# Performance work log

Measured on AMD Instinct MI355X. Metric: run time of the kernel, lower is better.

## Reference

```python
import jax, jax.numpy as jnp
from jax import lax
import numpy as np

START = 1  # strings_utils.SpecialSymbol.START
B, T, H, V = 16, 256, 512, 32000


def setup_inputs() -> dict:
    key = jax.random.key(0)
    ks = jax.random.split(key, 8)
    s = 0.05
    return {
        "hidden0": jax.random.normal(ks[0], (1, B, H), jnp.float32),
        "target": jax.random.randint(ks[1], (B, T), 0, V, jnp.int32),
        "E": jax.random.normal(ks[2], (V, H), jnp.float32) * s,
        "W_ih": jax.random.normal(ks[3], (3 * H, H), jnp.float32) * s,
        "W_hh": jax.random.normal(ks[4], (3 * H, H), jnp.float32) * s,
        "b_ih": jax.random.normal(ks[5], (3 * H,), jnp.float32) * s,
        "b_hh": jax.random.normal(ks[6], (3 * H,), jnp.float32) * s,
        "b_out": jax.random.normal(ks[7], (V,), jnp.float32) * s,
    }


def reference(hidden0, target, E, W_ih, W_hh, b_ih, b_hh, b_out):
    # Teacher forcing: step 0 feeds START, step di>0 feeds target[:, di-1]
    b, t = target.shape
    start = jnp.full((b, 1), START, dtype=target.dtype)
    step_tok = jnp.concatenate([start, target[:, :-1]], axis=1).T  # [T, B]
    h0 = hidden0[0]  # num_layers == 1 -> [B, H]

    def step(h, tok):
        x = E[tok]                                # [B, H] embedding gather
        gi = x @ W_ih.T + b_ih                    # [B, 3H]
        gh = h @ W_hh.T + b_hh                    # [B, 3H]
        i_r, i_z, i_n = jnp.split(gi, 3, axis=-1)
        h_r, h_z, h_n = jnp.split(gh, 3, axis=-1)
        r = jax.nn.sigmoid(i_r + h_r)
        z = jax.nn.sigmoid(i_z + h_z)
        n = jnp.tanh(i_n + r * h_n)
        h_new = (1.0 - z) * n + z * h             # [B, H]
        logits = h_new @ E.T + b_out              # tied-weight output [B, V]
        return h_new, logits

    _, logits = lax.scan(step, h0, step_tok)      # [T, B, V]
    return jnp.transpose(logits, (1, 0, 2))       # [B, T, V]
```

## Files before the change

kernel.cpp:

```cpp
#include <hip/hip_runtime.h>
#include <hip/hip_bf16.h>
#include <math.h>

#define Bq 16
#define Tq 256
#define Hq 512
#define Vq 32000
#define Gq 1536
#define NWG 16
#define LBLK 240
#define NBI 167

typedef __attribute__((ext_vector_type(8))) short short8;
typedef __attribute__((ext_vector_type(4))) float f32x4;
typedef __attribute__((ext_vector_type(4))) unsigned int u32x4;
typedef unsigned long long u64;

typedef const __attribute__((address_space(1))) void g_void;
typedef __attribute__((address_space(3))) void l_void;

__device__ __forceinline__ unsigned short f2bf(float f) {
    union { float f; unsigned int u; } v; v.f = f;
    unsigned int r = v.u + 0x7fffu + ((v.u >> 16) & 1u);
    return (unsigned short)(r >> 16);
}
__device__ __forceinline__ float bf2f(unsigned short h) {
    union { unsigned int u; float f; } v; v.u = ((unsigned int)h) << 16;
    return v.f;
}
__device__ __forceinline__ float sigm(float x) { return 1.0f / (1.0f + __expf(-x)); }
__device__ __forceinline__ float tanh_fast(float x) {
    float e = __expf(-2.0f * x);
    return (1.0f - e) / (1.0f + e);
}

__global__ void prep_kernel(const float* __restrict__ E, const float* __restrict__ Wih,
                            const float* __restrict__ Whh,
                            unsigned short* __restrict__ Ebf,
                            unsigned short* __restrict__ WihHi, unsigned short* __restrict__ WihLo,
                            unsigned short* __restrict__ WhhHi, unsigned short* __restrict__ WhhLo,
                            int* __restrict__ flags) {
    long tid = (long)blockIdx.x * blockDim.x + threadIdx.x;
    long stride = (long)gridDim.x * blockDim.x;
    for (long i = tid; i < (long)Vq * Hq; i += stride) Ebf[i] = f2bf(E[i]);
    for (long i = tid; i < (long)Gq * Hq; i += stride) {
        float w = Wih[i]; unsigned short hi = f2bf(w);
        WihHi[i] = hi; WihLo[i] = f2bf(w - bf2f(hi));
        w = Whh[i]; hi = f2bf(w);
        WhhHi[i] = hi; WhhLo[i] = f2bf(w - bf2f(hi));
    }
    if (tid < 2048) flags[tid] = 0;
}

__launch_bounds__(384)
__global__ void gi_kernel(const int* __restrict__ target, const float* __restrict__ E,
                          const unsigned short* __restrict__ WihHi,
                          const unsigned short* __restrict__ WihLo,
                          const float* __restrict__ b_ih, float* __restrict__ gi_all) {
    __shared__ __align__(16) unsigned short Ahi[16][520];
    __shared__ __align__(16) unsigned short Alo[16][520];
    __shared__ int toks[16];
    int t = blockIdx.x, gb = blockIdx.y;
    int tid = threadIdx.x;
    if (tid < 16) toks[tid] = (t == 0) ? 1 : target[tid * Tq + (t - 1)];
    __syncthreads();
    for (int idx = tid; idx < 16 * Hq; idx += 384) {
        int r = idx >> 9, k = idx & 511;
        float v = E[(long)toks[r] * Hq + k];
        unsigned short hi = f2bf(v);
        Ahi[r][k] = hi; Alo[r][k] = f2bf(v - bf2f(hi));
    }
    __syncthreads();
    int wave = tid >> 6, lane = tid & 63;
    int gcb = gb * 96 + wave * 16;
    int row = lane & 15, kg = (lane >> 4) * 8;
    const unsigned short* bh = WihHi + (long)(gcb + row) * Hq;
    const unsigned short* bl = WihLo + (long)(gcb + row) * Hq;
    f32x4 aHH = {0,0,0,0}, aHL = {0,0,0,0}, aLH = {0,0,0,0};
#pragma unroll
    for (int ks = 0; ks < 16; ++ks) {
        int k0 = ks * 32 + kg;
        short8 ah = *(const short8*)&Ahi[row][k0];
        short8 al = *(const short8*)&Alo[row][k0];
        short8 wh = *(const short8*)&bh[k0];
        short8 wl = *(const short8*)&bl[k0];
        aHH = __builtin_amdgcn_mfma_f32_16x16x32_bf16(ah, wh, aHH, 0, 0, 0);
        aHL = __builtin_amdgcn_mfma_f32_16x16x32_bf16(ah, wl, aHL, 0, 0, 0);
        aLH = __builtin_amdgcn_mfma_f32_16x16x32_bf16(al, wh, aLH, 0, 0, 0);
    }
    int g = gcb + row;
    float bi = b_ih[g];
#pragma unroll
    for (int q = 0; q < 4; ++q) {
        int b = (lane >> 4) * 4 + q;
        gi_all[((long)(t * 16 + b)) * Gq + g] = aHH[q] + aHL[q] + aLH[q] + bi;
    }
}

__launch_bounds__(384, 1)
__global__ void fused_kernel(const float* __restrict__ h0,
                             const unsigned short* __restrict__ WhhHi,
                             const unsigned short* __restrict__ WhhLo,
                             const float* __restrict__ b_hh,
                             const float* __restrict__ gi_all,
                             unsigned int* Hpk, u64* ring,
                             int* flags,
                             const unsigned short* __restrict__ Ebf,
                             const float* __restrict__ b_out,
                             float* __restrict__ out) {
    __shared__ __align__(16) char smem[41984];
    int tid = threadIdx.x, lane = tid & 63;

    if (blockIdx.x < NWG) {
        __builtin_amdgcn_s_setprio(1);
        unsigned short (*Ahi)[520] = (unsigned short (*)[520])smem;
        float (*gbuf)[16][33] = (float (*)[16][33])(smem + 16640);
        int w = blockIdx.x;
        int wave = tid >> 6;
        int gate = wave >> 1;
        int gcol = gate * 512 + w * 32 + (wave & 1) * 16;
        int row = lane & 15, kg = (lane >> 4) * 8;
        const unsigned short* bhp = WhhHi + (long)(gcol + row) * Hq;
        const unsigned short* blp = WhhLo + (long)(gcol + row) * Hq;
        short8 Bh[16], Bl[16];
#pragma unroll
        for (int ks = 0; ks < 16; ++ks) {
            Bh[ks] = *(const short8*)&bhp[ks * 32 + kg];
            Bl[ks] = *(const short8*)&blp[ks * 32 + kg];
        }
        float bhh = b_hh[gcol + row];
        float gin[4];
#pragma unroll
        for (int q = 0; q < 4; ++q) {
            int b = (lane >> 4) * 4 + q;
            gin[q] = gi_all[(long)b * Gq + (gcol + row)];
        }
        for (int t = 0; t < Tq; ++t) {
            if (t == 0) {
                for (int idx = tid; idx < Bq * Hq; idx += 384)
                    Ahi[idx >> 9][idx & 511] = f2bf(h0[idx]);
            } else {
                const u64* src = ring + ((t - 1) & 1) * 4096;
                u64 A0 = (u64)(src + tid);
                u64 A1 = (u64)(src + tid + 384);
                u64 A2 = (u64)(src + tid + 768);
                u64 A3 = (u64)(src + tid + 1152);
                u64 A4 = (u64)(src + tid + 1536);
                u64 A5 = (u64)(src + tid + 1920);
                u64 A6 = (u64)(src + tid + 2304);
                u64 A7 = (u64)(src + tid + 2688);
                u64 A8 = (u64)(src + tid + 3072);
                u64 A9 = (u64)(src + tid + 3456);
                u64 A10 = (u64)(src + ((tid < 256) ? (3840 + tid) : tid));
                u64 v0, v1, v2, v3, v4, v5, v6, v7, v8, v9, v10;
                unsigned int st = (unsigned int)t;
                int guard = 0;
                bool ok;
                do {
                    asm volatile(
                        "global_load_dwordx2 %0, %11, off sc0 sc1\n\t"
                        "global_load_dwordx2 %1, %12, off sc0 sc1\n\t"
                        "global_load_dwordx2 %2, %13, off sc0 sc1\n\t"
                        "global_load_dwordx2 %3, %14, off sc0 sc1\n\t"
                        "global_load_dwordx2 %4, %15, off sc0 sc1\n\t"
                        "global_load_dwordx2 %5, %16, off sc0 sc1\n\t"
                        "global_load_dwordx2 %6, %17, off sc0 sc1\n\t"
                        "global_load_dwordx2 %7, %18, off sc0 sc1\n\t"
                        "global_load_dwordx2 %8, %19, off sc0 sc1\n\t"
                        "global_load_dwordx2 %9, %20, off sc0 sc1\n\t"
                        "global_load_dwordx2 %10, %21, off sc0 sc1\n\t"
                        "s_waitcnt vmcnt(0)"
                        : "=&v"(v0), "=&v"(v1), "=&v"(v2), "=&v"(v3), "=&v"(v4),
                          "=&v"(v5), "=&v"(v6), "=&v"(v7), "=&v"(v8), "=&v"(v9),
                          "=&v"(v10)
                        : "v"(A0), "v"(A1), "v"(A2), "v"(A3), "v"(A4), "v"(A5),
                          "v"(A6), "v"(A7), "v"(A8), "v"(A9), "v"(A10)
                        : "memory");
                    bool mine = ((unsigned int)(v0 >> 32) == st) &&
                                ((unsigned int)(v1 >> 32) == st) &&
                                ((unsigned int)(v2 >> 32) == st) &&
                                ((unsigned int)(v3 >> 32) == st) &&
                                ((unsigned int)(v4 >> 32) == st) &&
                                ((unsigned int)(v5 >> 32) == st) &&
                                ((unsigned int)(v6 >> 32) == st) &&
                                ((unsigned int)(v7 >> 32) == st) &&
                                ((unsigned int)(v8 >> 32) == st) &&
                                ((unsigned int)(v9 >> 32) == st) &&
                                ((unsigned int)(v10 >> 32) == st);
                    ok = __all(mine);
                } while (!ok && ++guard < (1 << 15));
                {
                    int wv = tid;
                    *(unsigned int*)&Ahi[wv >> 8][(wv & 255) * 2] = (unsigned int)v0;
                    wv = tid + 384;
                    *(unsigned int*)&Ahi[wv >> 8][(wv & 255) * 2] = (unsigned int)v1;
                    wv = tid + 768;
                    *(unsigned int*)&Ahi[wv >> 8][(wv & 255) * 2] = (unsigned int)v2;
                    wv = tid + 1152;
                    *(unsigned int*)&Ahi[wv >> 8][(wv & 255) * 2] = (unsigned int)v3;
                    wv = tid + 1536;
                    *(unsigned int*)&Ahi[wv >> 8][(wv & 255) * 2] = (unsigned int)v4;
                    wv = tid + 1920;
                    *(unsigned int*)&Ahi[wv >> 8][(wv & 255) * 2] = (unsigned int)v5;
                    wv = tid + 2304;
                    *(unsigned int*)&Ahi[wv >> 8][(wv & 255) * 2] = (unsigned int)v6;
                    wv = tid + 2688;
                    *(unsigned int*)&Ahi[wv >> 8][(wv & 255) * 2] = (unsigned int)v7;
                    wv = tid + 3072;
                    *(unsigned int*)&Ahi[wv >> 8][(wv & 255) * 2] = (unsigned int)v8;
                    wv = tid + 3456;
                    *(unsigned int*)&Ahi[wv >> 8][(wv & 255) * 2] = (unsigned int)v9;
                    if (tid < 256) {
                        wv = 3840 + tid;
                        *(unsigned int*)&Ahi[wv >> 8][(wv & 255) * 2] = (unsigned int)v10;
                    }
                }
            }
            __syncthreads();
            f32x4 xH = {0,0,0,0}, xL = {0,0,0,0};
            f32x4 yH = {0,0,0,0}, yL = {0,0,0,0};
#pragma unroll
            for (int ks = 0; ks < 8; ++ks) {
                short8 ah = *(const short8*)&Ahi[row][ks * 32 + kg];
                xH = __builtin_amdgcn_mfma_f32_16x16x32_bf16(ah, Bh[ks], xH, 0, 0, 0);
                xL = __builtin_amdgcn_mfma_f32_16x16x32_bf16(ah, Bl[ks], xL, 0, 0, 0);
            }
#pragma unroll
            for (int ks = 8; ks < 16; ++ks) {
                short8 ah = *(const short8*)&Ahi[row][ks * 32 + kg];
                yH = __builtin_amdgcn_mfma_f32_16x16x32_bf16(ah, Bh[ks], yH, 0, 0, 0);
                yL = __builtin_amdgcn_mfma_f32_16x16x32_bf16(ah, Bl[ks], yL, 0, 0, 0);
            }
            int jj = (wave & 1) * 16 + row;
#pragma unroll
            for (int q = 0; q < 4; ++q) {
                int b = (lane >> 4) * 4 + q;
                float ghv = (xH[q] + yH[q]) + (xL[q] + yL[q]) + bhh;
                if (gate < 2) gbuf[gate][b][jj] = ghv + gin[q];
                else { gbuf[2][b][jj] = gin[q]; gbuf[3][b][jj] = ghv; }
            }
            __syncthreads();
            if (tid < 256) {
                int b = tid >> 4, jp = tid & 15;
                int j0 = jp * 2, j1 = j0 + 1;
                int jc0 = w * 32 + j0;
                float r0 = sigm(gbuf[0][b][j0]);
                float z0 = sigm(gbuf[1][b][j0]);
                float n0 = tanh_fast(gbuf[2][b][j0] + r0 * gbuf[3][b][j0]);
                float hn0 = (1.0f - z0) * n0 + z0 * bf2f(Ahi[b][jc0]);
                float r1 = sigm(gbuf[0][b][j1]);
                float z1 = sigm(gbuf[1][b][j1]);
                float n1 = tanh_fast(gbuf[2][b][j1] + r1 * gbuf[3][b][j1]);
                float hn1 = (1.0f - z1) * n1 + z1 * bf2f(Ahi[b][jc0 + 1]);
                unsigned int pk = (unsigned int)f2bf(hn0) |
                                  ((unsigned int)f2bf(hn1) << 16);
                long idx = b * 256 + w * 16 + jp;
                u64 word = ((u64)(unsigned int)(t + 1) << 32) | pk;
                __hip_atomic_store(&ring[(t & 1) * 4096 + idx], word,
                                   __ATOMIC_RELAXED, __HIP_MEMORY_SCOPE_AGENT);
                __hip_atomic_store(&Hpk[(long)t * 4096 + idx], pk,
                                   __ATOMIC_RELAXED, __HIP_MEMORY_SCOPE_AGENT);
                if ((t & 7) == 7) {
                    asm volatile("s_waitcnt vmcnt(0)" ::: "memory");
                    if (lane == 0)
                        __hip_atomic_store(&flags[(w * 4 + wave) * 32], t + 1,
                                           __ATOMIC_RELAXED, __HIP_MEMORY_SCOPE_AGENT);
                }
            }
            int tp = (t + 1 < Tq) ? (t + 1) : t;
#pragma unroll
            for (int q = 0; q < 4; ++q) {
                int b = (lane >> 4) * 4 + q;
                gin[q] = gi_all[((long)(tp * 16 + b)) * Gq + (gcol + row)];
            }
        }
    } else {
        unsigned short* As = (unsigned short*)smem;
        unsigned short* Bs = As + 128 * 64;
        int j = blockIdx.x - NWG;
        int s = (j < NBI) ? j : (j - NBI);
        int mlo = 0, mhi = 32;
        if (s < 73) { if (j < NBI) mhi = 16; else mlo = 16; }
        int n0 = s * 192;
        int d8 = 8 * (s & 1);
        int wid = tid >> 6;
        int wr = wid & 1, wc = wid >> 1;
        int fr = lane & 15, r7 = lane & 7, sb = lane >> 4;
        int rA = lane >> 3, slp = (lane & 7) ^ rA;
        for (int mt = mlo; mt < mhi; ++mt) {
            int m0 = mt * 128;
            if (tid < 64) {
                int need = (mt + 1) * 8 + d8;
                if (need > 256) need = 256;
                int guard = 0;
                while (guard < (1 << 18)) {
                    int fv = __hip_atomic_load(&flags[lane * 32], __ATOMIC_RELAXED,
                                               __HIP_MEMORY_SCOPE_AGENT);
                    if (__all(fv >= need)) break;
                    __builtin_amdgcn_s_sleep(127);
                    ++guard;
                }
            }
            __syncthreads();
            f32x4 acc[4][4] = {};
            const unsigned int* srcA = Hpk + (long)(mt * 8) * 4096;
            for (int kt = 0; kt < 8; ++kt) {
                if (kt) __syncthreads();
                int ko = kt * 64;
#pragma unroll
                for (int i = 0; i < 4; ++i) {
                    int brow = n0 + wid * 8 + i * 48 + rA;
                    if (brow > Vq - 1) brow = Vq - 1;
                    __builtin_amdgcn_global_load_lds(
                        (g_void*)(Ebf + (long)brow * Hq + ko + slp * 8),
                        (l_void*)(Bs + (wid * 8 + i * 48) * 64), 16, 0, 0);
                }
                for (int c = tid; c < 1024; c += 384) {
                    int r = c >> 3, g8 = c & 7;
                    u32x4 v = *(const u32x4*)&srcA[(long)(r >> 4) * 4096 +
                                                   (r & 15) * 256 + kt * 32 + g8 * 4];
                    *(u32x4*)&As[r * 64 + ((g8 ^ (r & 7)) << 3)] = v;
                }
                __syncthreads();
#pragma unroll
                for (int ks = 0; ks < 2; ++ks) {
                    short8 af[4], bfr[4];
#pragma unroll
                    for (int f = 0; f < 4; ++f) {
                        af[f]  = *(const short8*)&As[(wr * 64 + f * 16 + fr) * 64 +
                                                     (((sb + ks * 4) ^ r7) << 3)];
                        bfr[f] = *(const short8*)&Bs[(wc * 64 + f * 16 + fr) * 64 +
                                                     (((sb + ks * 4) ^ r7) << 3)];
                    }
#pragma unroll
                    for (int fm = 0; fm < 4; ++fm)
#pragma unroll
                        for (int fn = 0; fn < 4; ++fn)
                            acc[fm][fn] = __builtin_amdgcn_mfma_f32_16x16x32_bf16(
                                af[fm], bfr[fn], acc[fm][fn], 0, 0, 0);
                }
            }
#pragma unroll
            for (int fn = 0; fn < 4; ++fn) {
                int v = n0 + wc * 64 + fn * 16 + fr;
                if (v < Vq) {
                    float bo = b_out[v];
#pragma unroll
                    for (int fm = 0; fm < 4; ++fm) {
#pragma unroll
                        for (int q = 0; q < 4; ++q) {
                            int m = m0 + wr * 64 + fm * 16 + (lane >> 4) * 4 + q;
                            out[((long)(m & 15) * Tq + (m >> 4)) * Vq + v] =
                                acc[fm][fn][q] + bo;
                        }
                    }
                }
            }
        }
    }
}

extern "C" void kernel_launch(void* const* d_in, const int* in_sizes, int n_in,
                              void* d_out, int out_size, void* d_ws, size_t ws_size,
                              hipStream_t stream) {
    const float* h0    = (const float*)d_in[0];
    const int*   target= (const int*)d_in[1];
    const float* E     = (const float*)d_in[2];
    const float* Wih   = (const float*)d_in[3];
    const float* Whh   = (const float*)d_in[4];
    const float* b_ih  = (const float*)d_in[5];
    const float* b_hh  = (const float*)d_in[6];
    const float* b_out = (const float*)d_in[7];
    float* out = (float*)d_out;

    char* ws = (char*)d_ws;
    size_t off = 0;
    unsigned short* Ebf   = (unsigned short*)(ws + off); off += (size_t)Vq * Hq * 2;
    unsigned short* WihHi = (unsigned short*)(ws + off); off += (size_t)Gq * Hq * 2;
    unsigned short* WihLo = (unsigned short*)(ws + off); off += (size_t)Gq * Hq * 2;
    unsigned short* WhhHi = (unsigned short*)(ws + off); off += (size_t)Gq * Hq * 2;
    unsigned short* WhhLo = (unsigned short*)(ws + off); off += (size_t)Gq * Hq * 2;
    float*          gi_all= (float*)(ws + off);          off += (size_t)Tq * Bq * Gq * 4;
    unsigned int*   Hpk   = (unsigned int*)(ws + off);   off += (size_t)Tq * 4096 * 4;
    u64*            ring  = (u64*)(ws + off);            off += (size_t)2 * 4096 * 8;
    int*            flags = (int*)(ws + off);            off += 2048 * 4;

    prep_kernel<<<dim3(2048), dim3(256), 0, stream>>>(E, Wih, Whh, Ebf, WihHi, WihLo,
                                                      WhhHi, WhhLo, flags);
    gi_kernel<<<dim3(Tq, 16), dim3(384), 0, stream>>>(target, E, WihHi, WihLo, b_ih, gi_all);
    fused_kernel<<<dim3(256), dim3(384), 0, stream>>>(h0, WhhHi, WhhLo, b_hh, gi_all,
                                                      Hpk, ring, flags, Ebf, b_out, out);
}
```

Baseline: 934.1 us.

## Fuse prep and input-projection kernels into one persistent mega kernel with flags

Removes the separate prep and gi kernels. Weights are converted to bf16 hi/lo on the fly inside the recurrence and projection blocks, and the 240 consumer blocks compute the input-gate projections themselves before converting their slice of E and running the vocab GEMM. Per-timestep completion counters let the recurrent blocks start as soon as their gi rows are ready. This overlaps the input-projection work with the serial GRU and cuts launches and intermediate weight buffers. In exchange it adds per-element conversion work and extra spin-wait polling, and the serial path now waits on consumer progress.

After: 871.4 us. -6.7%, faster.

```diff
diff --git a/kernel.cpp b/kernel.cpp
--- a/kernel.cpp
+++ b/kernel.cpp
@@ -8,7 +8,7 @@
 #define Vq 32000
 #define Gq 1536
 #define NWG 16
-#define LBLK 240
+#define CONS 240
 #define NBI 167
 
 typedef __attribute__((ext_vector_type(8))) short short8;
@@ -34,80 +34,26 @@
     return (1.0f - e) / (1.0f + e);
 }
 
-__global__ void prep_kernel(const float* __restrict__ E, const float* __restrict__ Wih,
+__global__ void zero_kernel(int* __restrict__ flags, int* __restrict__ gicol) {
+    int tid = threadIdx.x;
+    for (int i = tid; i < 2048; i += 384) flags[i] = 0;
+    for (int i = tid; i < 256; i += 384) gicol[i] = 0;
+}
+
+__launch_bounds__(384, 1)
+__global__ void mega_kernel(const float* __restrict__ h0,
+                            const int* __restrict__ target,
+                            const float* __restrict__ E,
+                            const float* __restrict__ Wih,
                             const float* __restrict__ Whh,
+                            const float* __restrict__ b_ih,
+                            const float* __restrict__ b_hh,
+                            const float* __restrict__ b_out,
+                            float* gi_all,
+                            unsigned int* Hpk, u64* ring,
+                            int* flags, int* gicol,
                             unsigned short* __restrict__ Ebf,
-                            unsigned short* __restrict__ WihHi, unsigned short* __restrict__ WihLo,
-                            unsigned short* __restrict__ WhhHi, unsigned short* __restrict__ WhhLo,
-                            int* __restrict__ flags) {
-    long tid = (long)blockIdx.x * blockDim.x + threadIdx.x;
-    long stride = (long)gridDim.x * blockDim.x;
-    for (long i = tid; i < (long)Vq * Hq; i += stride) Ebf[i] = f2bf(E[i]);
-    for (long i = tid; i < (long)Gq * Hq; i += stride) {
-        float w = Wih[i]; unsigned short hi = f2bf(w);
-        WihHi[i] = hi; WihLo[i] = f2bf(w - bf2f(hi));
-        w = Whh[i]; hi = f2bf(w);
-        WhhHi[i] = hi; WhhLo[i] = f2bf(w - bf2f(hi));
-    }
-    if (tid < 2048) flags[tid] = 0;
-}
-
-__launch_bounds__(384)
-__global__ void gi_kernel(const int* __restrict__ target, const float* __restrict__ E,
-                          const unsigned short* __restrict__ WihHi,
-                          const unsigned short* __restrict__ WihLo,
-                          const float* __restrict__ b_ih, float* __restrict__ gi_all) {
-    __shared__ __align__(16) unsigned short Ahi[16][520];
-    __shared__ __align__(16) unsigned short Alo[16][520];
-    __shared__ int toks[16];
-    int t = blockIdx.x, gb = blockIdx.y;
-    int tid = threadIdx.x;
-    if (tid < 16) toks[tid] = (t == 0) ? 1 : target[tid * Tq + (t - 1)];
-    __syncthreads();
-    for (int idx = tid; idx < 16 * Hq; idx += 384) {
-        int r = idx >> 9, k = idx & 511;
-        float v = E[(long)toks[r] * Hq + k];
-        unsigned short hi = f2bf(v);
-        Ahi[r][k] = hi; Alo[r][k] = f2bf(v - bf2f(hi));
-    }
-    __syncthreads();
-    int wave = tid >> 6, lane = tid & 63;
-    int gcb = gb * 96 + wave * 16;
-    int row = lane & 15, kg = (lane >> 4) * 8;
-    const unsigned short* bh = WihHi + (long)(gcb + row) * Hq;
-    const unsigned short* bl = WihLo + (long)(gcb + row) * Hq;
-    f32x4 aHH = {0,0,0,0}, aHL = {0,0,0,0}, aLH = {0,0,0,0};
-#pragma unroll
-    for (int ks = 0; ks < 16; ++ks) {
-        int k0 = ks * 32 + kg;
-        short8 ah = *(const short8*)&Ahi[row][k0];
-        short8 al = *(const short8*)&Alo[row][k0];
-        short8 wh = *(const short8*)&bh[k0];
-        short8 wl = *(const short8*)&bl[k0];
-        aHH = __builtin_amdgcn_mfma_f32_16x16x32_bf16(ah, wh, aHH, 0, 0, 0);
-        aHL = __builtin_amdgcn_mfma_f32_16x16x32_bf16(ah, wl, aHL, 0, 0, 0);
-        aLH = __builtin_amdgcn_mfma_f32_16x16x32_bf16(al, wh, aLH, 0, 0, 0);
-    }
-    int g = gcb + row;
-    float bi = b_ih[g];
-#pragma unroll
-    for (int q = 0; q < 4; ++q) {
-        int b = (lane >> 4) * 4 + q;
-        gi_all[((long)(t * 16 + b)) * Gq + g] = aHH[q] + aHL[q] + aLH[q] + bi;
-    }
-}
-
-__launch_bounds__(384, 1)
-__global__ void fused_kernel(const float* __restrict__ h0,
-                             const unsigned short* __restrict__ WhhHi,
-                             const unsigned short* __restrict__ WhhLo,
-                             const float* __restrict__ b_hh,
-                             const float* __restrict__ gi_all,
-                             unsigned int* Hpk, u64* ring,
-                             int* flags,
-                             const unsigned short* __restrict__ Ebf,
-                             const float* __restrict__ b_out,
-                             float* __restrict__ out) {
+                            float* __restrict__ out) {
     __shared__ __align__(16) char smem[41984];
     int tid = threadIdx.x, lane = tid & 63;
 
@@ -120,15 +66,33 @@
         int gate = wave >> 1;
         int gcol = gate * 512 + w * 32 + (wave & 1) * 16;
         int row = lane & 15, kg = (lane >> 4) * 8;
-        const unsigned short* bhp = WhhHi + (long)(gcol + row) * Hq;
-        const unsigned short* blp = WhhLo + (long)(gcol + row) * Hq;
+        const float* whp = Whh + (long)(gcol + row) * Hq;
         short8 Bh[16], Bl[16];
 #pragma unroll
         for (int ks = 0; ks < 16; ++ks) {
-            Bh[ks] = *(const short8*)&bhp[ks * 32 + kg];
-            Bl[ks] = *(const short8*)&blp[ks * 32 + kg];
+            f32x4 a = *(const f32x4*)&whp[ks * 32 + kg];
+            f32x4 c = *(const f32x4*)&whp[ks * 32 + kg + 4];
+#pragma unroll
+            for (int e = 0; e < 4; ++e) {
+                unsigned short hi = f2bf(a[e]);
+                Bh[ks][e] = (short)hi; Bl[ks][e] = (short)f2bf(a[e] - bf2f(hi));
+                hi = f2bf(c[e]);
+                Bh[ks][e + 4] = (short)hi; Bl[ks][e + 4] = (short)f2bf(c[e] - bf2f(hi));
+            }
         }
         float bhh = b_hh[gcol + row];
+        {
+            int guard = 0;
+            while (guard < (1 << 20)) {
+                int g0 = __hip_atomic_load(&gicol[0], __ATOMIC_RELAXED,
+                                           __HIP_MEMORY_SCOPE_AGENT);
+                int g1 = __hip_atomic_load(&gicol[1], __ATOMIC_RELAXED,
+                                           __HIP_MEMORY_SCOPE_AGENT);
+                if (g0 >= 16 && g1 >= 16) break;
+                __builtin_amdgcn_s_sleep(8);
+                ++guard;
+            }
+        }
         float gin[4];
 #pragma unroll
         for (int q = 0; q < 4; ++q) {
@@ -152,29 +116,33 @@
                 u64 A8 = (u64)(src + tid + 3072);
                 u64 A9 = (u64)(src + tid + 3456);
                 u64 A10 = (u64)(src + ((tid < 256) ? (3840 + tid) : tid));
+                int tc = (t + 1 < Tq) ? (t + 1) : (Tq - 1);
+                u64 A11 = (u64)(gicol + tc);
                 u64 v0, v1, v2, v3, v4, v5, v6, v7, v8, v9, v10;
+                unsigned int g11;
                 unsigned int st = (unsigned int)t;
                 int guard = 0;
                 bool ok;
                 do {
                     asm volatile(
-                        "global_load_dwordx2 %0, %11, off sc0 sc1\n\t"
-                        "global_load_dwordx2 %1, %12, off sc0 sc1\n\t"
-                        "global_load_dwordx2 %2, %13, off sc0 sc1\n\t"
-                        "global_load_dwordx2 %3, %14, off sc0 sc1\n\t"
-                        "global_load_dwordx2 %4, %15, off sc0 sc1\n\t"
-                        "global_load_dwordx2 %5, %16, off sc0 sc1\n\t"
-                        "global_load_dwordx2 %6, %17, off sc0 sc1\n\t"
-                        "global_load_dwordx2 %7, %18, off sc0 sc1\n\t"
-                        "global_load_dwordx2 %8, %19, off sc0 sc1\n\t"
-                        "global_load_dwordx2 %9, %20, off sc0 sc1\n\t"
-                        "global_load_dwordx2 %10, %21, off sc0 sc1\n\t"
+                        "global_load_dwordx2 %0, %12, off sc0 sc1\n\t"
+                        "global_load_dwordx2 %1, %13, off sc0 sc1\n\t"
+                        "global_load_dwordx2 %2, %14, off sc0 sc1\n\t"
+                        "global_load_dwordx2 %3, %15, off sc0 sc1\n\t"
+                        "global_load_dwordx2 %4, %16, off sc0 sc1\n\t"
+                        "global_load_dwordx2 %5, %17, off sc0 sc1\n\t"
+                        "global_load_dwordx2 %6, %18, off sc0 sc1\n\t"
+                        "global_load_dwordx2 %7, %19, off sc0 sc1\n\t"
+                        "global_load_dwordx2 %8, %20, off sc0 sc1\n\t"
+                        "global_load_dwordx2 %9, %21, off sc0 sc1\n\t"
+                        "global_load_dwordx2 %10, %22, off sc0 sc1\n\t"
+                        "global_load_dword %11, %23, off sc0 sc1\n\t"
                         "s_waitcnt vmcnt(0)"
                         : "=&v"(v0), "=&v"(v1), "=&v"(v2), "=&v"(v3), "=&v"(v4),
                           "=&v"(v5), "=&v"(v6), "=&v"(v7), "=&v"(v8), "=&v"(v9),
-                          "=&v"(v10)
+                          "=&v"(v10), "=&v"(g11)
                         : "v"(A0), "v"(A1), "v"(A2), "v"(A3), "v"(A4), "v"(A5),
-                          "v"(A6), "v"(A7), "v"(A8), "v"(A9), "v"(A10)
+                          "v"(A6), "v"(A7), "v"(A8), "v"(A9), "v"(A10), "v"(A11)
                         : "memory");
                     bool mine = ((unsigned int)(v0 >> 32) == st) &&
                                 ((unsigned int)(v1 >> 32) == st) &&
@@ -186,8 +154,10 @@
                                 ((unsigned int)(v7 >> 32) == st) &&
                                 ((unsigned int)(v8 >> 32) == st) &&
                                 ((unsigned int)(v9 >> 32) == st) &&
-                                ((unsigned int)(v10 >> 32) == st);
+                                ((unsigned int)(v10 >> 32) == st) &&
+                                ((int)g11 >= 16);
                     ok = __all(mine);
+                    if (!ok) __builtin_amdgcn_s_sleep(1);
                 } while (!ok && ++guard < (1 << 15));
                 {
                     int wv = tid;
@@ -275,14 +245,80 @@
             }
         }
     } else {
+        int j = blockIdx.x - NWG;
+        int wave = tid >> 6;
+        int row = lane & 15, kg = (lane >> 4) * 8;
+        {
+            unsigned short (*Ahi)[520] = (unsigned short (*)[520])smem;
+            unsigned short (*Alo)[520] = (unsigned short (*)[520])(smem + 16640);
+            int* toks = (int*)(smem + 33280);
+            for (int item = j; item < 4096; item += CONS) {
+                int t = item >> 4, gb = item & 15;
+                __syncthreads();
+                if (tid < 16) toks[tid] = (t == 0) ? 1 : target[tid * Tq + (t - 1)];
+                __syncthreads();
+                for (int idx = tid; idx < 16 * Hq; idx += 384) {
+                    int r = idx >> 9, k = idx & 511;
+                    float v = E[(long)toks[r] * Hq + k];
+                    unsigned short hi = f2bf(v);
+                    Ahi[r][k] = hi; Alo[r][k] = f2bf(v - bf2f(hi));
+                }
+                __syncthreads();
+                int gcb = gb * 96 + wave * 16;
+                const float* wrow = Wih + (long)(gcb + row) * Hq;
+                f32x4 aHH = {0,0,0,0}, aHL = {0,0,0,0}, aLH = {0,0,0,0};
+#pragma unroll
+                for (int ks = 0; ks < 16; ++ks) {
+                    int k0 = ks * 32 + kg;
+                    short8 ah = *(const short8*)&Ahi[row][k0];
+                    short8 al = *(const short8*)&Alo[row][k0];
+                    f32x4 wa = *(const f32x4*)&wrow[k0];
+                    f32x4 wb = *(const f32x4*)&wrow[k0 + 4];
+                    short8 wh, wl;
+#pragma unroll
+                    for (int e = 0; e < 4; ++e) {
+                        unsigned short hi = f2bf(wa[e]);
+                        wh[e] = (short)hi; wl[e] = (short)f2bf(wa[e] - bf2f(hi));
+                        hi = f2bf(wb[e]);
+                        wh[e + 4] = (short)hi; wl[e + 4] = (short)f2bf(wb[e] - bf2f(hi));
+                    }
+                    aHH = __builtin_amdgcn_mfma_f32_16x16x32_bf16(ah, wh, aHH, 0, 0, 0);
+                    aHL = __builtin_amdgcn_mfma_f32_16x16x32_bf16(ah, wl, aHL, 0, 0, 0);
+                    aLH = __builtin_amdgcn_mfma_f32_16x16x32_bf16(al, wh, aLH, 0, 0, 0);
+                }
+                int g = gcb + row;
+                float bi = b_ih[g];
+#pragma unroll
+                for (int q = 0; q < 4; ++q) {
+                    int b = (lane >> 4) * 4 + q;
+                    __hip_atomic_store(&gi_all[((long)(t * 16 + b)) * Gq + g],
+                                       aHH[q] + aHL[q] + aLH[q] + bi,
+                                       __ATOMIC_RELAXED, __HIP_MEMORY_SCOPE_AGENT);
+                }
+                __syncthreads();
+                if (tid == 0)
+                    __hip_atomic_fetch_add(&gicol[t], 1, __ATOMIC_RELAXED,
+                                           __HIP_MEMORY_SCOPE_AGENT);
+            }
+        }
+        int s = (j < NBI) ? j : (j - NBI);
+        int n0 = s * 192;
+        int nend = (n0 + 192 < Vq) ? (n0 + 192) : Vq;
+        {
+            long base = (long)n0 * Hq;
+            long elems = (long)(nend - n0) * Hq;
+            for (long k = (long)tid * 4; k < elems; k += 384 * 4) {
+                f32x4 v = *(const f32x4*)&E[base + k];
+                unsigned short o0 = f2bf(v[0]), o1 = f2bf(v[1]);
+                unsigned short o2 = f2bf(v[2]), o3 = f2bf(v[3]);
+                *(u64*)&Ebf[base + k] = (u64)o0 | ((u64)o1 << 16) |
+                                        ((u64)o2 << 32) | ((u64)o3 << 48);
+            }
+        }
         unsigned short* As = (unsigned short*)smem;
         unsigned short* Bs = As + 128 * 64;
-        int j = blockIdx.x - NWG;
-        int s = (j < NBI) ? j : (j - NBI);
         int mlo = 0, mhi = 32;
         if (s < 73) { if (j < NBI) mhi = 16; else mlo = 16; }
-        int n0 = s * 192;
-        int d8 = 8 * (s & 1);
         int wid = tid >> 6;
         int wr = wid & 1, wc = wid >> 1;
         int fr = lane & 15, r7 = lane & 7, sb = lane >> 4;
@@ -290,8 +326,7 @@
         for (int mt = mlo; mt < mhi; ++mt) {
             int m0 = mt * 128;
             if (tid < 64) {
-                int need = (mt + 1) * 8 + d8;
-                if (need > 256) need = 256;
+                int need = (mt + 1) * 8;
                 int guard = 0;
                 while (guard < (1 << 18)) {
                     int fv = __hip_atomic_load(&flags[lane * 32], __ATOMIC_RELAXED,
@@ -376,18 +411,14 @@
     char* ws = (char*)d_ws;
     size_t off = 0;
     unsigned short* Ebf   = (unsigned short*)(ws + off); off += (size_t)Vq * Hq * 2;
-    unsigned short* WihHi = (unsigned short*)(ws + off); off += (size_t)Gq * Hq * 2;
-    unsigned short* WihLo = (unsigned short*)(ws + off); off += (size_t)Gq * Hq * 2;
-    unsigned short* WhhHi = (unsigned short*)(ws + off); off += (size_t)Gq * Hq * 2;
-    unsigned short* WhhLo = (unsigned short*)(ws + off); off += (size_t)Gq * Hq * 2;
     float*          gi_all= (float*)(ws + off);          off += (size_t)Tq * Bq * Gq * 4;
     unsigned int*   Hpk   = (unsigned int*)(ws + off);   off += (size_t)Tq * 4096 * 4;
     u64*            ring  = (u64*)(ws + off);            off += (size_t)2 * 4096 * 8;
     int*            flags = (int*)(ws + off);            off += 2048 * 4;
-
-    prep_kernel<<<dim3(2048), dim3(256), 0, stream>>>(E, Wih, Whh, Ebf, WihHi, WihLo,
-                                                      WhhHi, WhhLo, flags);
-    gi_kernel<<<dim3(Tq, 16), dim3(384), 0, stream>>>(target, E, WihHi, WihLo, b_ih, gi_all);
-    fused_kernel<<<dim3(256), dim3(384), 0, stream>>>(h0, WhhHi, WhhLo, b_hh, gi_all,
-                                                      Hpk, ring, flags, Ebf, b_out, out);
-}
+    int*            gicol = (int*)(ws + off);            off += 256 * 4;
+
+    zero_kernel<<<dim3(1), dim3(384), 0, stream>>>(flags, gicol);
+    mega_kernel<<<dim3(256), dim3(384), 0, stream>>>(h0, target, E, Wih, Whh, b_ih,
+                                                     b_hh, b_out, gi_all, Hpk, ring,
+                                                     flags, gicol, Ebf, out);
+}
```

## Fuse weight prep and input-gate GEMM into the persistent recurrent kernel

Applied to the files above, without the earlier changes.

Removes the separate prep and gi kernels. The 16 recurrent workgroups now convert W_hh and W_ih to hi/lo bf16 pairs in registers and compute the input-gate projection each step from embeddings prefetched during the previous step. The consumer blocks convert their own slice of E to bf16 before starting the logits GEMM. This cuts launch overhead and the gi_all round trip through global memory, and lets the E conversion overlap the recurrence. In exchange the serial recurrent step carries three extra MFMA chains, the consumer-side ordering changes (the d8 offset is dropped), and register pressure rises.

Result: slower. 2.756 ms (+195.1%).

```diff
diff --git a/kernel.cpp b/kernel.cpp
--- a/kernel.cpp
+++ b/kernel.cpp
@@ -8,7 +8,7 @@
 #define Vq 32000
 #define Gq 1536
 #define NWG 16
-#define LBLK 240
+#define CONS 240
 #define NBI 167
 
 typedef __attribute__((ext_vector_type(8))) short short8;
@@ -34,112 +34,92 @@
     return (1.0f - e) / (1.0f + e);
 }
 
-__global__ void prep_kernel(const float* __restrict__ E, const float* __restrict__ Wih,
+__global__ void zero_kernel(int* __restrict__ flags) {
+    int tid = threadIdx.x;
+    for (int i = tid; i < 2048; i += 384) flags[i] = 0;
+}
+
+__launch_bounds__(384, 1)
+__global__ void mega_kernel(const float* __restrict__ h0,
+                            const int* __restrict__ target,
+                            const float* __restrict__ E,
+                            const float* __restrict__ Wih,
                             const float* __restrict__ Whh,
+                            const float* __restrict__ b_ih,
+                            const float* __restrict__ b_hh,
+                            const float* __restrict__ b_out,
+                            unsigned int* Hpk, u64* ring,
+                            int* flags,
                             unsigned short* __restrict__ Ebf,
-                            unsigned short* __restrict__ WihHi, unsigned short* __restrict__ WihLo,
-                            unsigned short* __restrict__ WhhHi, unsigned short* __restrict__ WhhLo,
-                            int* __restrict__ flags) {
-    long tid = (long)blockIdx.x * blockDim.x + threadIdx.x;
-    long stride = (long)gridDim.x * blockDim.x;
-    for (long i = tid; i < (long)Vq * Hq; i += stride) Ebf[i] = f2bf(E[i]);
-    for (long i = tid; i < (long)Gq * Hq; i += stride) {
-        float w = Wih[i]; unsigned short hi = f2bf(w);
-        WihHi[i] = hi; WihLo[i] = f2bf(w - bf2f(hi));
-        w = Whh[i]; hi = f2bf(w);
-        WhhHi[i] = hi; WhhLo[i] = f2bf(w - bf2f(hi));
-    }
-    if (tid < 2048) flags[tid] = 0;
-}
-
-__launch_bounds__(384)
-__global__ void gi_kernel(const int* __restrict__ target, const float* __restrict__ E,
-                          const unsigned short* __restrict__ WihHi,
-                          const unsigned short* __restrict__ WihLo,
-                          const float* __restrict__ b_ih, float* __restrict__ gi_all) {
-    __shared__ __align__(16) unsigned short Ahi[16][520];
-    __shared__ __align__(16) unsigned short Alo[16][520];
-    __shared__ int toks[16];
-    int t = blockIdx.x, gb = blockIdx.y;
-    int tid = threadIdx.x;
-    if (tid < 16) toks[tid] = (t == 0) ? 1 : target[tid * Tq + (t - 1)];
-    __syncthreads();
-    for (int idx = tid; idx < 16 * Hq; idx += 384) {
-        int r = idx >> 9, k = idx & 511;
-        float v = E[(long)toks[r] * Hq + k];
-        unsigned short hi = f2bf(v);
-        Ahi[r][k] = hi; Alo[r][k] = f2bf(v - bf2f(hi));
-    }
-    __syncthreads();
-    int wave = tid >> 6, lane = tid & 63;
-    int gcb = gb * 96 + wave * 16;
-    int row = lane & 15, kg = (lane >> 4) * 8;
-    const unsigned short* bh = WihHi + (long)(gcb + row) * Hq;
-    const unsigned short* bl = WihLo + (long)(gcb + row) * Hq;
-    f32x4 aHH = {0,0,0,0}, aHL = {0,0,0,0}, aLH = {0,0,0,0};
-#pragma unroll
-    for (int ks = 0; ks < 16; ++ks) {
-        int k0 = ks * 32 + kg;
-        short8 ah = *(const short8*)&Ahi[row][k0];
-        short8 al = *(const short8*)&Alo[row][k0];
-        short8 wh = *(const short8*)&bh[k0];
-        short8 wl = *(const short8*)&bl[k0];
-        aHH = __builtin_amdgcn_mfma_f32_16x16x32_bf16(ah, wh, aHH, 0, 0, 0);
-        aHL = __builtin_amdgcn_mfma_f32_16x16x32_bf16(ah, wl, aHL, 0, 0, 0);
-        aLH = __builtin_amdgcn_mfma_f32_16x16x32_bf16(al, wh, aLH, 0, 0, 0);
-    }
-    int g = gcb + row;
-    float bi = b_ih[g];
-#pragma unroll
-    for (int q = 0; q < 4; ++q) {
-        int b = (lane >> 4) * 4 + q;
-        gi_all[((long)(t * 16 + b)) * Gq + g] = aHH[q] + aHL[q] + aLH[q] + bi;
-    }
-}
-
-__launch_bounds__(384, 1)
-__global__ void fused_kernel(const float* __restrict__ h0,
-                             const unsigned short* __restrict__ WhhHi,
-                             const unsigned short* __restrict__ WhhLo,
-                             const float* __restrict__ b_hh,
-                             const float* __restrict__ gi_all,
-                             unsigned int* Hpk, u64* ring,
-                             int* flags,
-                             const unsigned short* __restrict__ Ebf,
-                             const float* __restrict__ b_out,
-                             float* __restrict__ out) {
-    __shared__ __align__(16) char smem[41984];
+                            float* __restrict__ out) {
+    __shared__ __align__(16) char smem[58368];
     int tid = threadIdx.x, lane = tid & 63;
 
     if (blockIdx.x < NWG) {
         __builtin_amdgcn_s_setprio(1);
         unsigned short (*Ahi)[520] = (unsigned short (*)[520])smem;
-        float (*gbuf)[16][33] = (float (*)[16][33])(smem + 16640);
+        unsigned short (*Ehi)[520] = (unsigned short (*)[520])(smem + 16640);
+        unsigned short (*Elo)[520] = (unsigned short (*)[520])(smem + 33280);
+        float (*gbuf)[16][33] = (float (*)[16][33])(smem + 49920);
         int w = blockIdx.x;
         int wave = tid >> 6;
         int gate = wave >> 1;
         int gcol = gate * 512 + w * 32 + (wave & 1) * 16;
         int row = lane & 15, kg = (lane >> 4) * 8;
-        const unsigned short* bhp = WhhHi + (long)(gcol + row) * Hq;
-        const unsigned short* blp = WhhLo + (long)(gcol + row) * Hq;
-        short8 Bh[16], Bl[16];
+        const float* whp = Whh + (long)(gcol + row) * Hq;
+        const float* wip = Wih + (long)(gcol + row) * Hq;
+        short8 Bh[16], Bl[16], Ch[16], Cl[16];
 #pragma unroll
         for (int ks = 0; ks < 16; ++ks) {
-            Bh[ks] = *(const short8*)&bhp[ks * 32 + kg];
-            Bl[ks] = *(const short8*)&blp[ks * 32 + kg];
+            f32x4 a = *(const f32x4*)&whp[ks * 32 + kg];
+            f32x4 c = *(const f32x4*)&whp[ks * 32 + kg + 4];
+            f32x4 d = *(const f32x4*)&wip[ks * 32 + kg];
+            f32x4 e = *(const f32x4*)&wip[ks * 32 + kg + 4];
+#pragma unroll
+            for (int q = 0; q < 4; ++q) {
+                unsigned short hi = f2bf(a[q]);
+                Bh[ks][q] = (short)hi; Bl[ks][q] = (short)f2bf(a[q] - bf2f(hi));
+                hi = f2bf(c[q]);
+                Bh[ks][q + 4] = (short)hi; Bl[ks][q + 4] = (short)f2bf(c[q] - bf2f(hi));
+                hi = f2bf(d[q]);
+                Ch[ks][q] = (short)hi; Cl[ks][q] = (short)f2bf(d[q] - bf2f(hi));
+                hi = f2bf(e[q]);
+                Ch[ks][q + 4] = (short)hi; Cl[ks][q + 4] = (short)f2bf(e[q] - bf2f(hi));
+            }
         }
         float bhh = b_hh[gcol + row];
-        float gin[4];
-#pragma unroll
-        for (int q = 0; q < 4; ++q) {
-            int b = (lane >> 4) * 4 + q;
-            gin[q] = gi_all[(long)b * Gq + (gcol + row)];
+        float bih = b_ih[gcol + row];
+        for (int idx = tid; idx < Bq * Hq; idx += 384) {
+            int b = idx >> 9, k = idx & 511;
+            float v = E[512 + k];
+            unsigned short hi = f2bf(v);
+            Ehi[b][k] = hi; Elo[b][k] = f2bf(v - bf2f(hi));
         }
+        f32x4 er[6];
         for (int t = 0; t < Tq; ++t) {
             if (t == 0) {
                 for (int idx = tid; idx < Bq * Hq; idx += 384)
                     Ahi[idx >> 9][idx & 511] = f2bf(h0[idx]);
             } else {
+#pragma unroll
+                for (int i = 0; i < 5; ++i) {
+                    int c = tid + i * 384;
+                    int b = c >> 7, k = (c & 127) * 4;
+#pragma unroll
+                    for (int q = 0; q < 4; ++q) {
+                        unsigned short hi = f2bf(er[i][q]);
+                        Ehi[b][k + q] = hi; Elo[b][k + q] = f2bf(er[i][q] - bf2f(hi));
+                    }
+                }
+                if (tid < 128) {
+                    int c = 1920 + tid;
+                    int b = c >> 7, k = (c & 127) * 4;
+#pragma unroll
+                    for (int q = 0; q < 4; ++q) {
+                        unsigned short hi = f2bf(er[5][q]);
+                        Ehi[b][k + q] = hi; Elo[b][k + q] = f2bf(er[5][q] - bf2f(hi));
+                    }
+                }
                 const u64* src = ring + ((t - 1) & 1) * 4096;
                 u64 A0 = (u64)(src + tid);
                 u64 A1 = (u64)(src + tid + 384);
@@ -188,6 +168,7 @@
                                 ((unsigned int)(v9 >> 32) == st) &&
                                 ((unsigned int)(v10 >> 32) == st);
                     ok = __all(mine);
+                    if (!ok) __builtin_amdgcn_s_sleep(1);
                 } while (!ok && ++guard < (1 << 15));
                 {
                     int wv = tid;
@@ -219,25 +200,37 @@
             __syncthreads();
             f32x4 xH = {0,0,0,0}, xL = {0,0,0,0};
             f32x4 yH = {0,0,0,0}, yL = {0,0,0,0};
+            f32x4 gHH = {0,0,0,0}, gHL = {0,0,0,0}, gLH = {0,0,0,0};
 #pragma unroll
             for (int ks = 0; ks < 8; ++ks) {
                 short8 ah = *(const short8*)&Ahi[row][ks * 32 + kg];
                 xH = __builtin_amdgcn_mfma_f32_16x16x32_bf16(ah, Bh[ks], xH, 0, 0, 0);
                 xL = __builtin_amdgcn_mfma_f32_16x16x32_bf16(ah, Bl[ks], xL, 0, 0, 0);
+                short8 eh = *(const short8*)&Ehi[row][ks * 32 + kg];
+                short8 el = *(const short8*)&Elo[row][ks * 32 + kg];
+                gHH = __builtin_amdgcn_mfma_f32_16x16x32_bf16(eh, Ch[ks], gHH, 0, 0, 0);
+                gHL = __builtin_amdgcn_mfma_f32_16x16x32_bf16(eh, Cl[ks], gHL, 0, 0, 0);
+                gLH = __builtin_amdgcn_mfma_f32_16x16x32_bf16(el, Ch[ks], gLH, 0, 0, 0);
             }
 #pragma unroll
             for (int ks = 8; ks < 16; ++ks) {
                 short8 ah = *(const short8*)&Ahi[row][ks * 32 + kg];
                 yH = __builtin_amdgcn_mfma_f32_16x16x32_bf16(ah, Bh[ks], yH, 0, 0, 0);
                 yL = __builtin_amdgcn_mfma_f32_16x16x32_bf16(ah, Bl[ks], yL, 0, 0, 0);
+                short8 eh = *(const short8*)&Ehi[row][ks * 32 + kg];
+                short8 el = *(const short8*)&Elo[row][ks * 32 + kg];
+                gHH = __builtin_amdgcn_mfma_f32_16x16x32_bf16(eh, Ch[ks], gHH, 0, 0, 0);
+                gHL = __builtin_amdgcn_mfma_f32_16x16x32_bf16(eh, Cl[ks], gHL, 0, 0, 0);
+                gLH = __builtin_amdgcn_mfma_f32_16x16x32_bf16(el, Ch[ks], gLH, 0, 0, 0);
             }
             int jj = (wave & 1) * 16 + row;
 #pragma unroll
             for (int q = 0; q < 4; ++q) {
                 int b = (lane >> 4) * 4 + q;
                 float ghv = (xH[q] + yH[q]) + (xL[q] + yL[q]) + bhh;
-                if (gate < 2) gbuf[gate][b][jj] = ghv + gin[q];
-                else { gbuf[2][b][jj] = gin[q]; gbuf[3][b][jj] = ghv; }
+                float ginq = gHH[q] + gHL[q] + gLH[q] + bih;
+                if (gate < 2) gbuf[gate][b][jj] = ghv + ginq;
+                else { gbuf[2][b][jj] = ginq; gbuf[3][b][jj] = ghv; }
             }
             __syncthreads();
             if (tid < 256) {
@@ -267,22 +260,52 @@
                                            __ATOMIC_RELAXED, __HIP_MEMORY_SCOPE_AGENT);
                 }
             }
-            int tp = (t + 1 < Tq) ? (t + 1) : t;
-#pragma unroll
-            for (int q = 0; q < 4; ++q) {
-                int b = (lane >> 4) * 4 + q;
-                gin[q] = gi_all[((long)(tp * 16 + b)) * Gq + (gcol + row)];
+            if (t + 1 < Tq) {
+#pragma unroll
+                for (int i = 0; i < 5; ++i) {
+                    int c = tid + i * 384;
+                    int b = c >> 7;
+                    int tok = target[b * Tq + t];
+                    er[i] = *(const f32x4*)&E[(long)tok * Hq + (c & 127) * 4];
+                }
+                if (tid < 128) {
+                    int c = 1920 + tid;
+                    int b = c >> 7;
+                    int tok = target[b * Tq + t];
+                    er[5] = *(const f32x4*)&E[(long)tok * Hq + (c & 127) * 4];
+                }
             }
         }
     } else {
-        unsigned short* As = (unsigned short*)smem;
-        unsigned short* Bs = As + 128 * 64;
         int j = blockIdx.x - NWG;
         int s = (j < NBI) ? j : (j - NBI);
         int mlo = 0, mhi = 32;
         if (s < 73) { if (j < NBI) mhi = 16; else mlo = 16; }
         int n0 = s * 192;
-        int d8 = 8 * (s & 1);
+        int nend = (n0 + 192 < Vq) ? (n0 + 192) : Vq;
+        if (j < NBI) {
+            long base = (long)n0 * Hq;
+            long elems = (long)(nend - n0) * Hq;
+            for (long k = (long)tid * 4; k < elems; k += 384 * 4) {
+                f32x4 v = *(const f32x4*)&E[base + k];
+                unsigned short o0 = f2bf(v[0]), o1 = f2bf(v[1]);
+                unsigned short o2 = f2bf(v[2]), o3 = f2bf(v[3]);
+                *(u64*)&Ebf[base + k] = (u64)o0 | ((u64)o1 << 16) |
+                                        ((u64)o2 << 32) | ((u64)o3 << 48);
+            }
+        } else {
+            long base = (long)n0 * Hq;
+            long elems = (long)(nend - n0) * Hq;
+            for (long k = (long)tid * 4; k < elems; k += 384 * 4) {
+                f32x4 v = *(const f32x4*)&E[base + k];
+                unsigned short o0 = f2bf(v[0]), o1 = f2bf(v[1]);
+                unsigned short o2 = f2bf(v[2]), o3 = f2bf(v[3]);
+                *(u64*)&Ebf[base + k] = (u64)o0 | ((u64)o1 << 16) |
+                                        ((u64)o2 << 32) | ((u64)o3 << 48);
+            }
+        }
+        unsigned short* As = (unsigned short*)smem;
+        unsigned short* Bs = As + 128 * 64;
         int wid = tid >> 6;
         int wr = wid & 1, wc = wid >> 1;
         int fr = lane & 15, r7 = lane & 7, sb = lane >> 4;
@@ -290,8 +313,7 @@
         for (int mt = mlo; mt < mhi; ++mt) {
             int m0 = mt * 128;
             if (tid < 64) {
-                int need = (mt + 1) * 8 + d8;
-                if (need > 256) need = 256;
+                int need = (mt + 1) * 8;
                 int guard = 0;
                 while (guard < (1 << 18)) {
                     int fv = __hip_atomic_load(&flags[lane * 32], __ATOMIC_RELAXED,
@@ -376,18 +398,12 @@
     char* ws = (char*)d_ws;
     size_t off = 0;
     unsigned short* Ebf   = (unsigned short*)(ws + off); off += (size_t)Vq * Hq * 2;
-    unsigned short* WihHi = (unsigned short*)(ws + off); off += (size_t)Gq * Hq * 2;
-    unsigned short* WihLo = (unsigned short*)(ws + off); off += (size_t)Gq * Hq * 2;
-    unsigned short* WhhHi = (unsigned short*)(ws + off); off += (size_t)Gq * Hq * 2;
-    unsigned short* WhhLo = (unsigned short*)(ws + off); off += (size_t)Gq * Hq * 2;
-    float*          gi_all= (float*)(ws + off);          off += (size_t)Tq * Bq * Gq * 4;
     unsigned int*   Hpk   = (unsigned int*)(ws + off);   off += (size_t)Tq * 4096 * 4;
     u64*            ring  = (u64*)(ws + off);            off += (size_t)2 * 4096 * 8;
     int*            flags = (int*)(ws + off);            off += 2048 * 4;
 
-    prep_kernel<<<dim3(2048), dim3(256), 0, stream>>>(E, Wih, Whh, Ebf, WihHi, WihLo,
-                                                      WhhHi, WhhLo, flags);
-    gi_kernel<<<dim3(Tq, 16), dim3(384), 0, stream>>>(target, E, WihHi, WihLo, b_ih, gi_all);
-    fused_kernel<<<dim3(256), dim3(384), 0, stream>>>(h0, WhhHi, WhhLo, b_hh, gi_all,
-                                                      Hpk, ring, flags, Ebf, b_out, out);
-}
+    zero_kernel<<<dim3(1), dim3(384), 0, stream>>>(flags);
+    mega_kernel<<<dim3(NWG + CONS), dim3(384), 0, stream>>>(h0, target, E, Wih, Whh,
+                                                            b_ih, b_hh, b_out,
+                                                            Hpk, ring, flags, Ebf, out);
+}
```
